# Kernel tuning notes

Hardware: AMD Instinct MI355X
Metric: run time of the kernel (lower is better)

Reference implementation:

```python
import jax, jax.numpy as jnp
import numpy as np

DIM = 2048
HEADS = 16
DIM_HEAD = 128
FF_INNER = DIM * 4
SCALE_BASE = 512
EPS = 1e-5


def setup_inputs() -> dict:
    key = jax.random.key(0)
    k1, k2, k3, k4 = jax.random.split(key, 4)
    fused_out = HEADS * DIM_HEAD + DIM_HEAD + DIM_HEAD + 2 * FF_INNER  # 18688
    x = jax.random.normal(k1, (2, 2048, DIM), dtype=jnp.float32)
    gamma = jnp.ones((DIM,), dtype=jnp.float32)
    W_fused = jax.random.normal(k2, (DIM, fused_out), dtype=jnp.float32) * 0.02
    W_attn_out = jax.random.normal(k3, (HEADS * DIM_HEAD, DIM), dtype=jnp.float32) * 0.02
    W_ff_out = jax.random.normal(k4, (FF_INNER, DIM), dtype=jnp.float32) * 0.02
    return {"x": x, "gamma": gamma, "W_fused": W_fused, "W_attn_out": W_attn_out, "W_ff_out": W_ff_out}


def _rotate_half(t):
    t1, t2 = jnp.split(t, 2, axis=-1)
    return jnp.concatenate((-t2, t1), axis=-1)


def _rotary(n, dtype):
    # RotaryEmbedding with use_xpos=True, scale_base=512
    half = DIM_HEAD // 2
    inv_freq = 1.0 / (10000.0 ** (jnp.arange(0, DIM_HEAD, 2, dtype=dtype) / DIM_HEAD))
    t = jnp.arange(n, dtype=dtype)
    freqs = jnp.einsum('i,j->ij', t, inv_freq)          # [n, half]
    freqs = jnp.concatenate((freqs, freqs), axis=-1)    # [n, dh]
    scale_vec = (jnp.arange(0, DIM_HEAD, 2, dtype=dtype) + 0.4 * DIM_HEAD) / (1.4 * DIM_HEAD)
    power = (t - n // 2) / SCALE_BASE
    scale = scale_vec[None, :] ** power[:, None]        # [n, half]
    scale = jnp.concatenate((scale, scale), axis=-1)    # [n, dh]
    return freqs, scale


def _apply_rope(pos, t, scale):
    return t * jnp.cos(pos) * scale + _rotate_half(t) * jnp.sin(pos) * scale


def reference(x, gamma, W_fused, W_attn_out, W_ff_out):
    b, n, d = x.shape
    # LayerNorm (beta fixed at zero)
    mu = jnp.mean(x, axis=-1, keepdims=True)
    var = jnp.var(x, axis=-1, keepdims=True)
    xn = (x - mu) * jax.lax.rsqrt(var + EPS) * gamma

    proj = xn @ W_fused
    attn_inner = HEADS * DIM_HEAD
    q = proj[..., :attn_inner]
    k = proj[..., attn_inner:attn_inner + DIM_HEAD]
    v = proj[..., attn_inner + DIM_HEAD:attn_inner + 2 * DIM_HEAD]
    ff = proj[..., attn_inner + 2 * DIM_HEAD:]

    q = q.reshape(b, n, HEADS, DIM_HEAD).transpose(0, 2, 1, 3)  # b h n d

    pos, scale = _rotary(n, x.dtype)
    q = _apply_rope(pos, q, scale)            # broadcasts [n,dh] over b,h
    k = _apply_rope(pos, k, 1.0 / scale)      # k is [b, n, dh]

    # multi-query attention, causal
    sim = jnp.einsum('bhid,bjd->bhij', q, k) * (DIM_HEAD ** -0.5)
    causal_mask = jnp.triu(jnp.ones((n, n), dtype=bool), 1)
    sim = jnp.where(causal_mask, jnp.finfo(sim.dtype).min, sim)
    attn = jax.nn.softmax(sim, axis=-1)
    out = jnp.einsum('bhij,bjd->bhid', attn, v)
    out = out.transpose(0, 2, 1, 3).reshape(b, n, attn_inner)
    attn_out = out @ W_attn_out

    # SwiGLU: chunk -> silu(gate) * x
    ff_x, ff_gate = jnp.split(ff, 2, axis=-1)
    ff_out = (jax.nn.silu(ff_gate) * ff_x) @ W_ff_out

    return attn_out + ff_out
```

## Files before the change

### kernel.cpp

```cpp
#include <hip/hip_runtime.h>

typedef __attribute__((ext_vector_type(8))) short short8;
typedef __attribute__((ext_vector_type(4))) float floatx4;
typedef __attribute__((ext_vector_type(8))) unsigned short ushort8;
typedef __attribute__((ext_vector_type(2))) unsigned int uint2v;

#define FOUT 18688
#define FFI  8192
#define CATW 10240

__device__ __forceinline__ float b2f(unsigned short u){
  union { unsigned int i; float f; } v; v.i = ((unsigned int)u) << 16; return v.f;
}
__device__ __forceinline__ unsigned short f2b(float f){
  union { float f; unsigned int i; } v; v.f = f;
  unsigned int r = v.i + 0x7FFFu + ((v.i >> 16) & 1u);
  return (unsigned short)(r >> 16);
}
__device__ __forceinline__ void gld_lds16(const void* g, void* l){
  __builtin_amdgcn_global_load_lds((const __attribute__((address_space(1))) void*)g,
                                   (__attribute__((address_space(3))) void*)l, 16, 0, 0);
}

__global__ __launch_bounds__(256) void ln_kernel(const float* __restrict__ x,
                                                 const float* __restrict__ gamma,
                                                 unsigned short* __restrict__ xn){
  int row = blockIdx.x;
  const float* xr = x + (size_t)row * 2048;
  int tid = threadIdx.x;
  float v[8]; float s = 0.f, s2 = 0.f;
#pragma unroll
  for(int i=0;i<8;i++){ float t = xr[tid + i*256]; v[i]=t; s+=t; s2+=t*t; }
#pragma unroll
  for(int off=32; off>=1; off>>=1){ s += __shfl_down(s, off, 64); s2 += __shfl_down(s2, off, 64); }
  __shared__ float red[8];
  int wv = tid>>6, ln_ = tid&63;
  if(ln_==0){ red[wv] = s; red[wv+4] = s2; }
  __syncthreads();
  s  = red[0]+red[1]+red[2]+red[3];
  s2 = red[4]+red[5]+red[6]+red[7];
  float mu  = s * (1.f/2048.f);
  float var = s2 * (1.f/2048.f) - mu*mu;
  float rstd = rsqrtf(var + 1e-5f);
#pragma unroll
  for(int i=0;i<8;i++){
    float o = (v[i]-mu)*rstd*gamma[tid + i*256];
    xn[(size_t)row*2048 + tid + i*256] = f2b(o);
  }
}

__global__ void tcast_kernel(const float* __restrict__ W, unsigned short* __restrict__ Wt,
                             int R, int C, int S, int O){
  __shared__ float t[32][33];
  int bx = blockIdx.x*32, by = blockIdx.y*32;
  int tx = threadIdx.x, ty = threadIdx.y;
#pragma unroll
  for(int i=0;i<4;i++) t[ty+i*8][tx] = W[(size_t)(by+ty+i*8)*C + bx+tx];
  __syncthreads();
#pragma unroll
  for(int i=0;i<4;i++) Wt[(size_t)(bx+ty+i*8)*S + O + by+tx] = f2b(t[tx][ty+i*8]);
}

__global__ void vtrans_kernel(const unsigned short* __restrict__ proj, unsigned short* __restrict__ vt){
  __shared__ unsigned short t[32][33];
  int b = blockIdx.z;
  int n0 = blockIdx.x*32, d0 = blockIdx.y*32;
  int tx = threadIdx.x, ty = threadIdx.y;
#pragma unroll
  for(int i=0;i<4;i++) t[ty+i*8][tx] = proj[(size_t)(b*2048 + n0+ty+i*8)*FOUT + 2176 + d0+tx];
  __syncthreads();
#pragma unroll
  for(int i=0;i<4;i++) vt[((size_t)b*128 + d0+ty+i*8)*2048 + n0+tx] = t[tx][ty+i*8];
}

__global__ __launch_bounds__(256) void rope_tab_kernel(floatx4* __restrict__ tab){
  int idx = blockIdx.x*256 + threadIdx.x;
  int i = idx >> 6, j = idx & 63;
  float fj = (float)j, fi = (float)i;
  float p = fi * powf(10000.f, -fj*(1.f/64.f));
  float c = cosf(p), s = sinf(p);
  float sv = (2.f*fj + 51.2f) * (1.f/179.2f);
  float pw = (fi - 1024.f) * (1.f/512.f);
  float sc = powf(sv, pw);
  const float att = 0.08838834764831843f;
  floatx4 o; o[0]=c*sc*att; o[1]=s*sc*att; o[2]=c/sc; o[3]=s/sc;
  tab[idx] = o;
}

__global__ __launch_bounds__(256) void rope_kernel(unsigned short* __restrict__ proj,
                                                   const floatx4* __restrict__ tab){
  int row = blockIdx.x;
  int i = row & 2047;
  unsigned short* pr = proj + (size_t)row*FOUT;
  for(int item = threadIdx.x; item < 17*64; item += 256){
    int slot = item >> 6;
    int j = item & 63;
    floatx4 t = tab[i*64 + j];
    float cs = (slot==16) ? t[2] : t[0];
    float ss = (slot==16) ? t[3] : t[1];
    int colbase = (slot<16) ? slot*128 : 2048;
    float x1 = b2f(pr[colbase+j]);
    float x2 = b2f(pr[colbase+j+64]);
    pr[colbase+j]    = f2b(x1*cs - x2*ss);
    pr[colbase+j+64] = f2b(x2*cs + x1*ss);
  }
}

#define SCHED0() __builtin_amdgcn_sched_barrier(0)
#define BARR()   do{ SCHED0(); __builtin_amdgcn_s_barrier(); SCHED0(); }while(0)

template<int MODE>
__global__ __launch_bounds__(512, 2) void gemm8p_kernel(const unsigned short* __restrict__ A,
                                                        const unsigned short* __restrict__ Bt,
                                                        unsigned short* __restrict__ Cb,
                                                        float* __restrict__ Cf,
                                                        int N, int K, int NT, int ntn,
                                                        size_t zstride){
  __shared__ unsigned short lds[65536];
  const int tid = threadIdx.x;
  const int wave = tid>>6, lane = tid&63;
  const int l15 = lane&15, l4 = lane>>4;
  const int wr = wave>>2, wc = wave&3;
  int id = blockIdx.x;
  int cpx = (int)gridDim.x >> 3;
  int swz = (id & 7)*cpx + (id >> 3);
  int tm = swz / ntn, tn = swz - tm*ntn;
  int kbase = (int)blockIdx.z * (NT*64);
  const unsigned short* Ab = A  + (size_t)tm*256*K + kbase;
  const unsigned short* Bb = Bt + (size_t)tn*256*K + kbase;
  if(MODE==1) Cf += (size_t)blockIdx.z * zstride;

  const int r0 = tid>>3;
  const int colc = ((tid&7) ^ (r0&7))*8;
  const int dstw = wave*512;

#define STAGE(t_, h_, isB_) do{ \
    const unsigned short* g_ = (isB_) ? Bb : Ab; \
    int db_ = (((t_)&1)<<15) + ((isB_)<<14) + ((h_)<<13) + dstw; \
    gld_lds16(g_ + (size_t)((h_)*128 + r0)*K + (t_)*64 + colc, &lds[db_]); \
    gld_lds16(g_ + (size_t)((h_)*128 + r0 + 64)*K + (t_)*64 + colc, &lds[db_ + 4096]); \
  }while(0)

  const int sw8 = l15&7;
  const int fo0 = ((l4    )^sw8)*8;
  const int fo1 = ((l4 + 4)^sw8)*8;
  const int albase = (wr*128 + l15)*64;
  const int blbase = 16384 + (wc*64 + l15)*64;

#define RD_A0(buf_, mf_, kk_) a0_[(mf_)*2+(kk_)] = *(const short8*)&lds[(buf_) + albase + (mf_)*1024 + ((kk_)?fo1:fo0)]
#define RD_A1(buf_, mf_, kk_) a1_[(mf_)*2+(kk_)] = *(const short8*)&lds[(buf_) + albase + 4096 + (mf_)*1024 + ((kk_)?fo1:fo0)]
#define RD_B(buf_, nf_, kk_)  b_[(nf_)*2+(kk_)]  = *(const short8*)&lds[(buf_) + blbase + (nf_)*1024 + ((kk_)?fo1:fo0)]
#define MFMA_Q(aarr_, mo_, no_) do{ \
  _Pragma("unroll") for(int kk=0; kk<2; kk++) \
  _Pragma("unroll") for(int mf=0; mf<4; mf++) \
  _Pragma("unroll") for(int nf=0; nf<2; nf++) \
    acc[(mo_)*4+mf][(no_)*2+nf] = __builtin_amdgcn_mfma_f32_16x16x32_bf16( \
      b_[((no_)*2+nf)*2+kk], aarr_[mf*2+kk], acc[(mo_)*4+mf][(no_)*2+nf], 0,0,0); \
}while(0)

  floatx4 acc[8][4];
#pragma unroll
  for(int i=0;i<8;i++)
#pragma unroll
    for(int j=0;j<4;j++) acc[i][j] = (floatx4)0.f;

  short8 a0_[8], a1_[8], b_[8];

  STAGE(0,0,0); STAGE(0,1,0); STAGE(0,0,1); STAGE(0,1,1);
  STAGE(1,0,1); STAGE(1,1,1); STAGE(1,0,0);
  asm volatile("s_waitcnt vmcnt(6)" ::: "memory");
  SCHED0();
  BARR();
#pragma unroll
  for(int mf=0; mf<4; mf++){ RD_A0(0,mf,0); RD_A0(0,mf,1); }
#pragma unroll
  for(int nf=0; nf<2; nf++){ RD_B(0,nf,0); RD_B(0,nf,1); }
  SCHED0();

  for(int t=0; t<NT; ++t){
    const int bufo = (t&1)<<15;
    const int nbuf = bufo ^ 32768;
    if(t+1 < NT) STAGE(t+1,1,0);
    BARR();
    RD_B(bufo,2,0); RD_B(bufo,2,1); RD_B(bufo,3,0); RD_B(bufo,3,1);
    asm volatile("s_waitcnt lgkmcnt(4)" ::: "memory");
    SCHED0();
    __builtin_amdgcn_s_setprio(1);
    MFMA_Q(a0_,0,0);
    __builtin_amdgcn_s_setprio(0);
    BARR();
    if(t+2 < NT) STAGE(t+2,0,1);
    BARR();
#pragma unroll
    for(int mf=0; mf<4; mf++){ RD_A1(bufo,mf,0); RD_A1(bufo,mf,1); }
    asm volatile("s_waitcnt lgkmcnt(8)" ::: "memory");
    SCHED0();
    __builtin_amdgcn_s_setprio(1);
    MFMA_Q(a0_,0,1);
    __builtin_amdgcn_s_setprio(0);
    BARR();
    if(t+2 < NT){
      STAGE(t+2,1,1);
      asm volatile("s_waitcnt vmcnt(8)" ::: "memory");
    } else if(t+1 < NT){
      asm volatile("s_waitcnt vmcnt(4)" ::: "memory");
    }
    SCHED0();
    BARR();
    asm volatile("s_waitcnt lgkmcnt(0)" ::: "memory");
    SCHED0();
    __builtin_amdgcn_s_setprio(1);
    MFMA_Q(a1_,1,0);
    __builtin_amdgcn_s_setprio(0);
    SCHED0();
    if(t+1 < NT){ RD_B(nbuf,0,0); RD_B(nbuf,0,1); RD_B(nbuf,1,0); RD_B(nbuf,1,1); }
    BARR();
    if(t+2 < NT){
      STAGE(t+2,0,0);
      asm volatile("s_waitcnt vmcnt(6)" ::: "memory");
    } else if(t+1 < NT){
      asm volatile("s_waitcnt vmcnt(0)" ::: "memory");
    }
    SCHED0();
    BARR();
    if(t+1 < NT){
#pragma unroll
      for(int mf=0; mf<4; mf++){ RD_A0(nbuf,mf,0); RD_A0(nbuf,mf,1); }
    }
    SCHED0();
    __builtin_amdgcn_s_setprio(1);
    MFMA_Q(a1_,1,1);
    __builtin_amdgcn_s_setprio(0);
    BARR();
  }

  const size_t crow0 = (size_t)tm*256 + wr*128 + l15;
  const size_t ccol0 = (size_t)tn*256 + wc*64 + l4*4;
#pragma unroll
  for(int mi=0; mi<8; mi++){
    size_t row = crow0 + (mi>>2)*64 + (mi&3)*16;
#pragma unroll
    for(int nj=0; nj<4; nj++){
      size_t col = ccol0 + nj*16;
      floatx4 v = acc[mi][nj];
      if(MODE==0){
        uint2v u;
        u[0] = (unsigned int)f2b(v[0]) | ((unsigned int)f2b(v[1])<<16);
        u[1] = (unsigned int)f2b(v[2]) | ((unsigned int)f2b(v[3])<<16);
        *(uint2v*)&Cb[row*N + col] = u;
      } else {
        *(floatx4*)&Cf[row*N + col] = v;
      }
    }
  }
}

__global__ __launch_bounds__(256) void add2_kernel(const float* __restrict__ p0,
                                                   const float* __restrict__ p1,
                                                   float* __restrict__ o, int n4){
  for(int i = blockIdx.x*256 + threadIdx.x; i < n4; i += gridDim.x*256){
    floatx4 a = ((const floatx4*)p0)[i];
    floatx4 b = ((const floatx4*)p1)[i];
    ((floatx4*)o)[i] = a + b;
  }
}

__global__ __launch_bounds__(256) void attn_kernel(const unsigned short* __restrict__ proj,
                                                   const unsigned short* __restrict__ vt,
                                                   unsigned short* __restrict__ ao){
  __shared__ unsigned short lK[64*128];
  __shared__ unsigned short lV[128*64];
  __shared__ unsigned short lP[4*16*64];
  int qt = blockIdx.x, hh = blockIdx.y, b = blockIdx.z;
  int tid = threadIdx.x, wave = tid>>6, lane = tid&63;
  int l15 = lane&15, l4 = lane>>4;
  int q0 = qt*64;
  int qrow = q0 + wave*16 + l15;
  const unsigned short* qp = proj + (size_t)(b*2048 + qrow)*FOUT + hh*128 + l4*8;
  short8 qf[4];
#pragma unroll
  for(int ds=0; ds<4; ds++) qf[ds] = *(const short8*)(qp + ds*32);
  floatx4 po[8];
#pragma unroll
  for(int dt=0; dt<8; dt++) po[dt] = (floatx4)0.f;
  float mrun[4] = {-1e30f,-1e30f,-1e30f,-1e30f};
  float lrun[4] = {0.f,0.f,0.f,0.f};
  unsigned short* lPw = lP + wave*1024;
  const unsigned short* kb = proj + (size_t)(b*2048)*FOUT + 2048;
  const unsigned short* vb = vt + (size_t)b*128*2048;

  for(int kv=0; kv<=qt; kv++){
    int kv0 = kv*64;
#pragma unroll
    for(int it=0; it<4; it++){
      int f = it*256 + tid;
      int r = f>>4, pc = f&15;
      int gc = pc ^ (r&7);
      gld_lds16(kb + (size_t)(kv0 + r)*FOUT + gc*8, &lK[(it*256 + wave*64)*8]);
    }
#pragma unroll
    for(int it=0; it<4; it++){
      int f = it*256 + tid;
      int d = f>>3, pc = f&7;
      int gc = pc ^ (d&7);
      gld_lds16(vb + (size_t)d*2048 + kv0 + gc*8, &lV[(it*256 + wave*64)*8]);
    }
    __syncthreads();
    floatx4 sa[4];
#pragma unroll
    for(int jt=0;jt<4;jt++) sa[jt] = (floatx4)0.f;
#pragma unroll
    for(int jt=0;jt<4;jt++){
      int krow = jt*16 + l15;
#pragma unroll
      for(int ds=0; ds<4; ds++){
        int pc = (l4 + ds*4) ^ (krow&7);
        short8 kf = *(const short8*)&lK[krow*128 + pc*8];
        sa[jt] = __builtin_amdgcn_mfma_f32_16x16x32_bf16(qf[ds], kf, sa[jt], 0,0,0);
      }
    }
    float pv[4][4];
    bool diag = (kv == qt);
#pragma unroll
    for(int jt=0;jt<4;jt++){
#pragma unroll
      for(int r=0;r<4;r++){
        float s = sa[jt][r];
        if(diag && (kv0 + jt*16 + l15 > q0 + wave*16 + l4*4 + r)) s = -1e30f;
        pv[jt][r] = s;
      }
    }
    float mnew[4], corr[4];
#pragma unroll
    for(int r=0;r<4;r++){
      float mx = fmaxf(fmaxf(pv[0][r],pv[1][r]),fmaxf(pv[2][r],pv[3][r]));
      mx = fmaxf(mx, __shfl_xor(mx, 1, 64));
      mx = fmaxf(mx, __shfl_xor(mx, 2, 64));
      mx = fmaxf(mx, __shfl_xor(mx, 4, 64));
      mx = fmaxf(mx, __shfl_xor(mx, 8, 64));
      float mn = fmaxf(mrun[r], mx);
      corr[r] = __expf(mrun[r] - mn);
      mrun[r] = mn;
      mnew[r] = mn;
    }
    float rsum[4] = {0.f,0.f,0.f,0.f};
#pragma unroll
    for(int jt=0;jt<4;jt++){
#pragma unroll
      for(int r=0;r<4;r++){
        float p = __expf(pv[jt][r] - mnew[r]);
        pv[jt][r] = p;
        rsum[r] += p;
      }
    }
#pragma unroll
    for(int r=0;r<4;r++){
      float rs = rsum[r];
      rs += __shfl_xor(rs, 1, 64);
      rs += __shfl_xor(rs, 2, 64);
      rs += __shfl_xor(rs, 4, 64);
      rs += __shfl_xor(rs, 8, 64);
      lrun[r] = lrun[r]*corr[r] + rs;
    }
#pragma unroll
    for(int dt=0;dt<8;dt++){
#pragma unroll
      for(int r=0;r<4;r++) po[dt][r] *= corr[r];
    }
#pragma unroll
    for(int jt=0;jt<4;jt++){
#pragma unroll
      for(int r=0;r<4;r++){
        int i_ = l4*4 + r;
        int j = jt*16 + l15;
        int pc = (j>>3) ^ (i_&7);
        lPw[i_*64 + pc*8 + (j&7)] = f2b(pv[jt][r]);
      }
    }
    asm volatile("s_waitcnt lgkmcnt(0)" ::: "memory");
    short8 pf[2];
#pragma unroll
    for(int ks=0;ks<2;ks++){
      int pc = (l4 + ks*4) ^ (l15&7);
      pf[ks] = *(const short8*)&lPw[l15*64 + pc*8];
    }
#pragma unroll
    for(int dt=0;dt<8;dt++){
      int d = dt*16 + l15;
#pragma unroll
      for(int ks=0;ks<2;ks++){
        int pc = (ks*4 + l4) ^ (d&7);
        short8 vf = *(const short8*)&lV[d*64 + pc*8];
        po[dt] = __builtin_amdgcn_mfma_f32_16x16x32_bf16(pf[ks], vf, po[dt], 0,0,0);
      }
    }
    __syncthreads();
  }
#pragma unroll
  for(int r=0;r<4;r++){
    float inv = 1.f / lrun[r];
    size_t orow = (size_t)(b*2048 + q0 + wave*16 + l4*4 + r);
#pragma unroll
    for(int dt=0;dt<8;dt++){
      ao[orow*CATW + hh*128 + dt*16 + l15] = f2b(po[dt][r]*inv);
    }
  }
}

__global__ __launch_bounds__(256) void swiglu_kernel(const unsigned short* __restrict__ proj,
                                                     unsigned short* __restrict__ cat){
  size_t idx = (size_t)blockIdx.x*256 + threadIdx.x;
  int row = (int)(idx >> 10);
  int c8  = (int)(idx & 1023);
  const unsigned short* pr = proj + (size_t)row*FOUT + 2304 + c8*8;
  ushort8 xv = *(const ushort8*)pr;
  ushort8 gv = *(const ushort8*)(pr + FFI);
  ushort8 ov;
#pragma unroll
  for(int e=0;e<8;e++){
    float xf = b2f(xv[e]);
    float gf = b2f(gv[e]);
    float sg = gf / (1.f + __expf(-gf));
    ov[e] = f2b(sg*xf);
  }
  *(ushort8*)(cat + (size_t)row*CATW + 2048 + c8*8) = ov;
}

extern "C" void kernel_launch(void* const* d_in, const int* in_sizes, int n_in,
                              void* d_out, int out_size, void* d_ws, size_t ws_size,
                              hipStream_t stream){
  const float* x     = (const float*)d_in[0];
  const float* gamma = (const float*)d_in[1];
  const float* Wf    = (const float*)d_in[2];
  const float* Wa    = (const float*)d_in[3];
  const float* Wff   = (const float*)d_in[4];
  float* out = (float*)d_out;

  char* p = (char*)d_ws;
  unsigned short* xn    = (unsigned short*)p;  p += (size_t)4096*2048*2;
  unsigned short* WfT   = (unsigned short*)p;  p += (size_t)18688*2048*2;
  unsigned short* proj  = (unsigned short*)p;  p += (size_t)4096*18688*2;
  unsigned short* BtCat = (unsigned short*)p;  p += (size_t)2048*CATW*2;
  unsigned short* cat   = (unsigned short*)p;  p += (size_t)4096*CATW*2;
  unsigned short* vtb   = (unsigned short*)p;  p += (size_t)2*128*2048*2;
  floatx4*        rtab  = (floatx4*)p;         p += (size_t)2048*64*16;
  float* part = (float*)d_ws;

  ln_kernel<<<4096, 256, 0, stream>>>(x, gamma, xn);
  rope_tab_kernel<<<512, 256, 0, stream>>>(rtab);
  tcast_kernel<<<dim3(584,64),  dim3(32,8), 0, stream>>>(Wf,  WfT,   2048, 18688, 2048, 0);
  tcast_kernel<<<dim3(64,64),   dim3(32,8), 0, stream>>>(Wa,  BtCat, 2048, 2048,  CATW, 0);
  tcast_kernel<<<dim3(64,256),  dim3(32,8), 0, stream>>>(Wff, BtCat, 8192, 2048,  CATW, 2048);
  gemm8p_kernel<0><<<dim3(1168,1,1), 512, 0, stream>>>(xn, WfT, proj, nullptr, 18688, 2048, 32, 73, 0);
  rope_kernel<<<4096, 256, 0, stream>>>(proj, rtab);
  vtrans_kernel<<<dim3(64,4,2), dim3(32,8), 0, stream>>>(proj, vtb);
  attn_kernel<<<dim3(32,16,2), 256, 0, stream>>>(proj, vtb, cat);
  swiglu_kernel<<<16384, 256, 0, stream>>>(proj, cat);
  gemm8p_kernel<1><<<dim3(128,1,2), 512, 0, stream>>>(cat, BtCat, nullptr, part, 2048, 10240, 80, 8,
                                                      (size_t)4096*2048);
  add2_kernel<<<2048, 256, 0, stream>>>(part, part + (size_t)4096*2048, out, 2097152);
}
```

Baseline: 861.1 us.

## Restructure GEMM main loop: drop cross-iteration LDS prefetch and sched barriers

Rewrites the software pipeline of the bf16 MFMA GEMM so each iteration loads its own A0/B fragments from LDS at the start, instead of prefetching the next buffer's fragments during the previous iteration. Removes most sched_barrier fences and the intermediate vmcnt waits around the third stage, relying on a full lgkmcnt(0) wait before each MFMA quarter. This simplifies the schedule and gives the compiler freedom, but exposes LDS read latency before the MFMAs and reduces LDS/MFMA overlap. Dropping the vmcnt wait after STAGE(t+2,1,1) may also risk reading data before global-to-LDS loads land.

```diff
diff --git a/kernel.cpp b/kernel.cpp
--- a/kernel.cpp
+++ b/kernel.cpp
@@ -105,9 +105,6 @@
     pr[colbase+j+64] = f2b(x2*cs + x1*ss);
   }
 }
-
-#define SCHED0() __builtin_amdgcn_sched_barrier(0)
-#define BARR()   do{ SCHED0(); __builtin_amdgcn_s_barrier(); SCHED0(); }while(0)
 
 template<int MODE>
 __global__ __launch_bounds__(512, 2) void gemm8p_kernel(const unsigned short* __restrict__ A,
@@ -157,6 +154,8 @@
     acc[(mo_)*4+mf][(no_)*2+nf] = __builtin_amdgcn_mfma_f32_16x16x32_bf16( \
       b_[((no_)*2+nf)*2+kk], aarr_[mf*2+kk], acc[(mo_)*4+mf][(no_)*2+nf], 0,0,0); \
 }while(0)
+#define LG0() do{ asm volatile("s_waitcnt lgkmcnt(0)" ::: "memory"); \
+                  __builtin_amdgcn_sched_barrier(0); }while(0)
 
   floatx4 acc[8][4];
 #pragma unroll
@@ -169,69 +168,49 @@
   STAGE(0,0,0); STAGE(0,1,0); STAGE(0,0,1); STAGE(0,1,1);
   STAGE(1,0,1); STAGE(1,1,1); STAGE(1,0,0);
   asm volatile("s_waitcnt vmcnt(6)" ::: "memory");
-  SCHED0();
-  BARR();
-#pragma unroll
-  for(int mf=0; mf<4; mf++){ RD_A0(0,mf,0); RD_A0(0,mf,1); }
-#pragma unroll
-  for(int nf=0; nf<2; nf++){ RD_B(0,nf,0); RD_B(0,nf,1); }
-  SCHED0();
+  __builtin_amdgcn_s_barrier();
 
   for(int t=0; t<NT; ++t){
     const int bufo = (t&1)<<15;
-    const int nbuf = bufo ^ 32768;
+#pragma unroll
+    for(int mf=0; mf<4; mf++){ RD_A0(bufo,mf,0); RD_A0(bufo,mf,1); }
+    RD_B(bufo,0,0); RD_B(bufo,0,1); RD_B(bufo,1,0); RD_B(bufo,1,1);
     if(t+1 < NT) STAGE(t+1,1,0);
-    BARR();
-    RD_B(bufo,2,0); RD_B(bufo,2,1); RD_B(bufo,3,0); RD_B(bufo,3,1);
-    asm volatile("s_waitcnt lgkmcnt(4)" ::: "memory");
-    SCHED0();
+    asm volatile("s_waitcnt lgkmcnt(8)" ::: "memory");
+    __builtin_amdgcn_s_barrier();
+    LG0();
     __builtin_amdgcn_s_setprio(1);
     MFMA_Q(a0_,0,0);
     __builtin_amdgcn_s_setprio(0);
-    BARR();
+    __builtin_amdgcn_s_barrier();
+    RD_B(bufo,2,0); RD_B(bufo,2,1); RD_B(bufo,3,0); RD_B(bufo,3,1);
     if(t+2 < NT) STAGE(t+2,0,1);
-    BARR();
-#pragma unroll
-    for(int mf=0; mf<4; mf++){ RD_A1(bufo,mf,0); RD_A1(bufo,mf,1); }
-    asm volatile("s_waitcnt lgkmcnt(8)" ::: "memory");
-    SCHED0();
+    __builtin_amdgcn_s_barrier();
+    LG0();
     __builtin_amdgcn_s_setprio(1);
     MFMA_Q(a0_,0,1);
     __builtin_amdgcn_s_setprio(0);
-    BARR();
-    if(t+2 < NT){
-      STAGE(t+2,1,1);
-      asm volatile("s_waitcnt vmcnt(8)" ::: "memory");
-    } else if(t+1 < NT){
-      asm volatile("s_waitcnt vmcnt(4)" ::: "memory");
-    }
-    SCHED0();
-    BARR();
-    asm volatile("s_waitcnt lgkmcnt(0)" ::: "memory");
-    SCHED0();
+    __builtin_amdgcn_s_barrier();
+#pragma unroll
+    for(int mf=0; mf<4; mf++){ RD_A1(bufo,mf,0); RD_A1(bufo,mf,1); }
+    if(t+2 < NT) STAGE(t+2,1,1);
+    __builtin_amdgcn_s_barrier();
+    LG0();
     __builtin_amdgcn_s_setprio(1);
     MFMA_Q(a1_,1,0);
     __builtin_amdgcn_s_setprio(0);
-    SCHED0();
-    if(t+1 < NT){ RD_B(nbuf,0,0); RD_B(nbuf,0,1); RD_B(nbuf,1,0); RD_B(nbuf,1,1); }
-    BARR();
+    __builtin_amdgcn_s_barrier();
     if(t+2 < NT){
       STAGE(t+2,0,0);
       asm volatile("s_waitcnt vmcnt(6)" ::: "memory");
     } else if(t+1 < NT){
       asm volatile("s_waitcnt vmcnt(0)" ::: "memory");
     }
-    SCHED0();
-    BARR();
-    if(t+1 < NT){
-#pragma unroll
-      for(int mf=0; mf<4; mf++){ RD_A0(nbuf,mf,0); RD_A0(nbuf,mf,1); }
-    }
-    SCHED0();
+    __builtin_amdgcn_s_barrier();
     __builtin_amdgcn_s_setprio(1);
     MFMA_Q(a1_,1,1);
     __builtin_amdgcn_s_setprio(0);
-    BARR();
+    __builtin_amdgcn_s_barrier();
   }
 
   const size_t crow0 = (size_t)tm*256 + wr*128 + l15;
```

New measurement: 842.8 us. -2.1%, faster.

## Add triple-buffered K=32 GEMM for output projection; simplify 8-phase GEMM pipeline

Applied to the files above, without the earlier changes.

Adds a new gemm3b kernel that uses 32-wide K tiles with three LDS buffers, one barrier per tile and prefetch two tiles ahead, and uses it for the split-K output projection GEMM. The first GEMM kernel is also restructured: LDS fragment reads for the next tile are no longer overlapped with the current tile's MFMAs, and the operand order and epilogue change to scalar per-element stores. The aim is a simpler, cheaper synchronisation schedule for the second GEMM. The trade-off is that the first GEMM loses its read/compute overlap and now writes scalars instead of vectors, which could slow it down.

```diff
diff --git a/kernel.cpp b/kernel.cpp
--- a/kernel.cpp
+++ b/kernel.cpp
@@ -21,6 +21,9 @@
   __builtin_amdgcn_global_load_lds((const __attribute__((address_space(1))) void*)g,
                                    (__attribute__((address_space(3))) void*)l, 16, 0, 0);
 }
+
+#define SCHED0() __builtin_amdgcn_sched_barrier(0)
+#define BARR()   do{ SCHED0(); __builtin_amdgcn_s_barrier(); SCHED0(); }while(0)
 
 __global__ __launch_bounds__(256) void ln_kernel(const float* __restrict__ x,
                                                  const float* __restrict__ gamma,
@@ -106,16 +109,12 @@
   }
 }
 
-#define SCHED0() __builtin_amdgcn_sched_barrier(0)
-#define BARR()   do{ SCHED0(); __builtin_amdgcn_s_barrier(); SCHED0(); }while(0)
-
 template<int MODE>
 __global__ __launch_bounds__(512, 2) void gemm8p_kernel(const unsigned short* __restrict__ A,
                                                         const unsigned short* __restrict__ Bt,
                                                         unsigned short* __restrict__ Cb,
                                                         float* __restrict__ Cf,
-                                                        int N, int K, int NT, int ntn,
-                                                        size_t zstride){
+                                                        int N, int K, int NT, int ntn){
   __shared__ unsigned short lds[65536];
   const int tid = threadIdx.x;
   const int wave = tid>>6, lane = tid&63;
@@ -125,10 +124,8 @@
   int cpx = (int)gridDim.x >> 3;
   int swz = (id & 7)*cpx + (id >> 3);
   int tm = swz / ntn, tn = swz - tm*ntn;
-  int kbase = (int)blockIdx.z * (NT*64);
-  const unsigned short* Ab = A  + (size_t)tm*256*K + kbase;
-  const unsigned short* Bb = Bt + (size_t)tn*256*K + kbase;
-  if(MODE==1) Cf += (size_t)blockIdx.z * zstride;
+  const unsigned short* Ab = A  + (size_t)tm*256*K;
+  const unsigned short* Bb = Bt + (size_t)tn*256*K;
 
   const int r0 = tid>>3;
   const int colc = ((tid&7) ^ (r0&7))*8;
@@ -147,15 +144,14 @@
   const int albase = (wr*128 + l15)*64;
   const int blbase = 16384 + (wc*64 + l15)*64;
 
-#define RD_A0(buf_, mf_, kk_) a0_[(mf_)*2+(kk_)] = *(const short8*)&lds[(buf_) + albase + (mf_)*1024 + ((kk_)?fo1:fo0)]
-#define RD_A1(buf_, mf_, kk_) a1_[(mf_)*2+(kk_)] = *(const short8*)&lds[(buf_) + albase + 4096 + (mf_)*1024 + ((kk_)?fo1:fo0)]
-#define RD_B(buf_, nf_, kk_)  b_[(nf_)*2+(kk_)]  = *(const short8*)&lds[(buf_) + blbase + (nf_)*1024 + ((kk_)?fo1:fo0)]
-#define MFMA_Q(aarr_, mo_, no_) do{ \
-  _Pragma("unroll") for(int kk=0; kk<2; kk++) \
+#define RD_A(buf_, mh_, mf_, kk_) a_[(mf_)*2+(kk_)] = *(const short8*)&lds[(buf_) + albase + (mh_)*4096 + (mf_)*1024 + ((kk_)?fo1:fo0)]
+#define RD_B(buf_, nf_, kk_)      b_[(nf_)*2+(kk_)]  = *(const short8*)&lds[(buf_) + blbase + (nf_)*1024 + ((kk_)?fo1:fo0)]
+#define MFMA_Q(mo_, no_) do{ \
   _Pragma("unroll") for(int mf=0; mf<4; mf++) \
   _Pragma("unroll") for(int nf=0; nf<2; nf++) \
+  _Pragma("unroll") for(int kk=0; kk<2; kk++) \
     acc[(mo_)*4+mf][(no_)*2+nf] = __builtin_amdgcn_mfma_f32_16x16x32_bf16( \
-      b_[((no_)*2+nf)*2+kk], aarr_[mf*2+kk], acc[(mo_)*4+mf][(no_)*2+nf], 0,0,0); \
+      a_[mf*2+kk], b_[((no_)*2+nf)*2+kk], acc[(mo_)*4+mf][(no_)*2+nf], 0,0,0); \
 }while(0)
 
   floatx4 acc[8][4];
@@ -163,57 +159,42 @@
   for(int i=0;i<8;i++)
 #pragma unroll
     for(int j=0;j<4;j++) acc[i][j] = (floatx4)0.f;
-
-  short8 a0_[8], a1_[8], b_[8];
 
   STAGE(0,0,0); STAGE(0,1,0); STAGE(0,0,1); STAGE(0,1,1);
   STAGE(1,0,1); STAGE(1,1,1); STAGE(1,0,0);
   asm volatile("s_waitcnt vmcnt(6)" ::: "memory");
-  SCHED0();
   BARR();
-#pragma unroll
-  for(int mf=0; mf<4; mf++){ RD_A0(0,mf,0); RD_A0(0,mf,1); }
-#pragma unroll
-  for(int nf=0; nf<2; nf++){ RD_B(0,nf,0); RD_B(0,nf,1); }
-  SCHED0();
-
+
+  short8 a_[8], b_[8];
   for(int t=0; t<NT; ++t){
     const int bufo = (t&1)<<15;
-    const int nbuf = bufo ^ 32768;
+#pragma unroll
+    for(int mf=0; mf<4; mf++){ RD_A(bufo,0,mf,0); RD_A(bufo,0,mf,1); }
+#pragma unroll
+    for(int nf=0; nf<4; nf++){ RD_B(bufo,nf,0); RD_B(bufo,nf,1); }
     if(t+1 < NT) STAGE(t+1,1,0);
     BARR();
-    RD_B(bufo,2,0); RD_B(bufo,2,1); RD_B(bufo,3,0); RD_B(bufo,3,1);
-    asm volatile("s_waitcnt lgkmcnt(4)" ::: "memory");
+    asm volatile("s_waitcnt lgkmcnt(0)" ::: "memory");
     SCHED0();
     __builtin_amdgcn_s_setprio(1);
-    MFMA_Q(a0_,0,0);
+    MFMA_Q(0,0);
     __builtin_amdgcn_s_setprio(0);
     BARR();
     if(t+2 < NT) STAGE(t+2,0,1);
     BARR();
-#pragma unroll
-    for(int mf=0; mf<4; mf++){ RD_A1(bufo,mf,0); RD_A1(bufo,mf,1); }
-    asm volatile("s_waitcnt lgkmcnt(8)" ::: "memory");
-    SCHED0();
     __builtin_amdgcn_s_setprio(1);
-    MFMA_Q(a0_,0,1);
+    MFMA_Q(0,1);
     __builtin_amdgcn_s_setprio(0);
     BARR();
-    if(t+2 < NT){
-      STAGE(t+2,1,1);
-      asm volatile("s_waitcnt vmcnt(8)" ::: "memory");
-    } else if(t+1 < NT){
-      asm volatile("s_waitcnt vmcnt(4)" ::: "memory");
-    }
-    SCHED0();
+#pragma unroll
+    for(int mf=0; mf<4; mf++){ RD_A(bufo,1,mf,0); RD_A(bufo,1,mf,1); }
+    if(t+2 < NT) STAGE(t+2,1,1);
     BARR();
     asm volatile("s_waitcnt lgkmcnt(0)" ::: "memory");
     SCHED0();
     __builtin_amdgcn_s_setprio(1);
-    MFMA_Q(a1_,1,0);
+    MFMA_Q(1,0);
     __builtin_amdgcn_s_setprio(0);
-    SCHED0();
-    if(t+1 < NT){ RD_B(nbuf,0,0); RD_B(nbuf,0,1); RD_B(nbuf,1,0); RD_B(nbuf,1,1); }
     BARR();
     if(t+2 < NT){
       STAGE(t+2,0,0);
@@ -223,26 +204,125 @@
     }
     SCHED0();
     BARR();
-    if(t+1 < NT){
-#pragma unroll
-      for(int mf=0; mf<4; mf++){ RD_A0(nbuf,mf,0); RD_A0(nbuf,mf,1); }
-    }
-    SCHED0();
     __builtin_amdgcn_s_setprio(1);
-    MFMA_Q(a1_,1,1);
+    MFMA_Q(1,1);
     __builtin_amdgcn_s_setprio(0);
-    BARR();
+    SCHED0();
+    BARR();
+  }
+
+  const size_t crow0 = (size_t)tm*256 + wr*64 + 0;
+  (void)crow0;
+#pragma unroll
+  for(int m=0;m<8;m++){
+#pragma unroll
+    for(int n=0;n<4;n++){
+#pragma unroll
+      for(int r=0;r<4;r++){
+        size_t row = (size_t)tm*256 + wr*128 + (m>>2)*64 + (m&3)*16 + l4*4 + r;
+        size_t col = (size_t)tn*256 + wc*64 + n*16 + l15;
+        float v = acc[m][n][r];
+        if(MODE==0)      Cb[row*N + col] = f2b(v);
+        else             Cf[row*N + col] = v;
+      }
+    }
+  }
+}
+
+template<int MODE>
+__global__ __launch_bounds__(512, 2) void gemm3b_kernel(const unsigned short* __restrict__ A,
+                                                        const unsigned short* __restrict__ Bt,
+                                                        unsigned short* __restrict__ Cb,
+                                                        float* __restrict__ Cf,
+                                                        int N, int K, int NT, int ntn,
+                                                        size_t zstride){
+  __shared__ unsigned short lds[49152];
+  const int tid = threadIdx.x;
+  const int wave = tid>>6, lane = tid&63;
+  const int l15 = lane&15, l4 = lane>>4;
+  const int wr = wave>>2, wc = wave&3;
+  int id = blockIdx.x;
+  int cpx = (int)gridDim.x >> 3;
+  int swz = (id & 7)*cpx + (id >> 3);
+  int tm = swz / ntn, tn = swz - tm*ntn;
+  int kbase = (int)blockIdx.z * (NT*32);
+  const unsigned short* Ab = A  + (size_t)tm*256*K + kbase;
+  const unsigned short* Bb = Bt + (size_t)tn*256*K + kbase;
+  if(MODE==1) Cf += (size_t)blockIdx.z * zstride;
+
+  const int r0 = tid>>2;
+  const int gcol = ((tid&3) ^ ((r0>>1)&3))*8;
+  const int dstl = wave*64*8;
+
+#define STG3(t_, isB_, bufo_) do{ \
+    const unsigned short* g_ = (isB_) ? Bb : Ab; \
+    int bo_ = (bufo_) + (isB_)*8192; \
+    gld_lds16(g_ + (size_t)(      r0)*K + (t_)*32 + gcol, &lds[bo_ +        dstl]); \
+    gld_lds16(g_ + (size_t)(128 + r0)*K + (t_)*32 + gcol, &lds[bo_ + 4096 + dstl]); \
+  }while(0)
+
+  const int fo = (l4 ^ ((l15>>1)&3))*8;
+  const int albase = (wr*128 + l15)*32;
+  const int blbase = 8192 + (wc*64 + l15)*32;
+
+  floatx4 acc[8][4];
+#pragma unroll
+  for(int i=0;i<8;i++)
+#pragma unroll
+    for(int j=0;j<4;j++) acc[i][j] = (floatx4)0.f;
+
+  short8 a_[8], b_[4];
+
+  STG3(0,0,0);     STG3(0,1,0);
+  STG3(1,0,16384); STG3(1,1,16384);
+
+  int bufo = 0, sbo = 32768;
+  for(int t=0; t<NT; ++t){
+    if(t+1 < NT){ asm volatile("s_waitcnt vmcnt(4)" ::: "memory"); }
+    else        { asm volatile("s_waitcnt vmcnt(0)" ::: "memory"); }
+    SCHED0();
+    asm volatile("s_barrier" ::: "memory");
+    SCHED0();
+#pragma unroll
+    for(int mf=0; mf<8; mf++) a_[mf] = *(const short8*)&lds[bufo + albase + mf*512 + fo];
+    b_[0] = *(const short8*)&lds[bufo + blbase +       fo];
+    b_[1] = *(const short8*)&lds[bufo + blbase + 512 + fo];
+    SCHED0();
+    if(t+2 < NT){ STG3(t+2,0,sbo); STG3(t+2,1,sbo); }
+    b_[2] = *(const short8*)&lds[bufo + blbase + 1024 + fo];
+    b_[3] = *(const short8*)&lds[bufo + blbase + 1536 + fo];
+    SCHED0();
+    asm volatile("s_waitcnt lgkmcnt(2)" ::: "memory");
+    SCHED0();
+    __builtin_amdgcn_s_setprio(1);
+#pragma unroll
+    for(int mf=0; mf<8; mf++)
+#pragma unroll
+      for(int nf=0; nf<2; nf++)
+        acc[mf][nf] = __builtin_amdgcn_mfma_f32_16x16x32_bf16(b_[nf], a_[mf], acc[mf][nf], 0,0,0);
+    __builtin_amdgcn_s_setprio(0);
+    asm volatile("s_waitcnt lgkmcnt(0)" ::: "memory");
+    SCHED0();
+    __builtin_amdgcn_s_setprio(1);
+#pragma unroll
+    for(int mf=0; mf<8; mf++)
+#pragma unroll
+      for(int nf=2; nf<4; nf++)
+        acc[mf][nf] = __builtin_amdgcn_mfma_f32_16x16x32_bf16(b_[nf], a_[mf], acc[mf][nf], 0,0,0);
+    __builtin_amdgcn_s_setprio(0);
+    bufo += 16384; if(bufo == 49152) bufo = 0;
+    sbo  += 16384; if(sbo  == 49152) sbo  = 0;
   }
 
   const size_t crow0 = (size_t)tm*256 + wr*128 + l15;
   const size_t ccol0 = (size_t)tn*256 + wc*64 + l4*4;
 #pragma unroll
-  for(int mi=0; mi<8; mi++){
-    size_t row = crow0 + (mi>>2)*64 + (mi&3)*16;
-#pragma unroll
-    for(int nj=0; nj<4; nj++){
-      size_t col = ccol0 + nj*16;
-      floatx4 v = acc[mi][nj];
+  for(int mf=0; mf<8; mf++){
+    size_t row = crow0 + mf*16;
+#pragma unroll
+    for(int nf=0; nf<4; nf++){
+      size_t col = ccol0 + nf*16;
+      floatx4 v = acc[mf][nf];
       if(MODE==0){
         uint2v u;
         u[0] = (unsigned int)f2b(v[0]) | ((unsigned int)f2b(v[1])<<16);
@@ -451,12 +531,12 @@
   tcast_kernel<<<dim3(584,64),  dim3(32,8), 0, stream>>>(Wf,  WfT,   2048, 18688, 2048, 0);
   tcast_kernel<<<dim3(64,64),   dim3(32,8), 0, stream>>>(Wa,  BtCat, 2048, 2048,  CATW, 0);
   tcast_kernel<<<dim3(64,256),  dim3(32,8), 0, stream>>>(Wff, BtCat, 8192, 2048,  CATW, 2048);
-  gemm8p_kernel<0><<<dim3(1168,1,1), 512, 0, stream>>>(xn, WfT, proj, nullptr, 18688, 2048, 32, 73, 0);
+  gemm8p_kernel<0><<<dim3(1168,1,1), 512, 0, stream>>>(xn, WfT, proj, nullptr, 18688, 2048, 32, 73);
   rope_kernel<<<4096, 256, 0, stream>>>(proj, rtab);
   vtrans_kernel<<<dim3(64,4,2), dim3(32,8), 0, stream>>>(proj, vtb);
   attn_kernel<<<dim3(32,16,2), 256, 0, stream>>>(proj, vtb, cat);
   swiglu_kernel<<<16384, 256, 0, stream>>>(proj, cat);
-  gemm8p_kernel<1><<<dim3(128,1,2), 512, 0, stream>>>(cat, BtCat, nullptr, part, 2048, 10240, 80, 8,
+  gemm3b_kernel<1><<<dim3(128,1,2), 512, 0, stream>>>(cat, BtCat, nullptr, part, 2048, 10240, 160, 8,
                                                       (size_t)4096*2048);
   add2_kernel<<<2048, 256, 0, stream>>>(part, part + (size_t)4096*2048, out, 2097152);
 }
```

New measurement: 841.1 us. 2.3% less time.
